# Kernel tuning notes

Measured on AMD Instinct MI355X. Metric: run time of the kernel, lower is better.

Reference implementation:

```python
import jax, jax.numpy as jnp
import numpy as np

VOCAB = 41      # len(MOL_DICT) + 1
EMB = 512       # EMBEDDING_SIZE
HID = 1024
B, T = 128, 256


def setup_inputs() -> dict:
    key = jax.random.key(0)
    ks = jax.random.split(key, 8)
    x = jax.random.randint(ks[0], (B, T), 0, VOCAB)
    # realistic prefix padding mask: True for valid tokens, False for padding
    lengths = jax.random.randint(ks[1], (B,), T // 4, T + 1)
    padding_mask = jnp.arange(T)[None, :] < lengths[:, None]
    s = 0.05
    emb_table = jax.random.normal(ks[2], (VOCAB, EMB), jnp.float32) * s
    gru_kernel = jax.random.normal(ks[3], (EMB, 3 * HID), jnp.float32) * s
    gru_rec_kernel = jax.random.normal(ks[4], (HID, 3 * HID), jnp.float32) * s
    gru_bias = jax.random.normal(ks[5], (2, 3 * HID), jnp.float32) * s
    dense_w = jax.random.normal(ks[6], (HID, VOCAB), jnp.float32) * s
    dense_b = jnp.zeros((VOCAB,), jnp.float32)
    return {"x": x, "padding_mask": padding_mask, "emb_table": emb_table,
            "gru_kernel": gru_kernel, "gru_rec_kernel": gru_rec_kernel,
            "gru_bias": gru_bias, "dense_w": dense_w, "dense_b": dense_b}


def _gru_scan(x_proj_t, mask_t, rec_kernel, rec_bias):
    # x_proj_t: [T, B, 3H] precomputed input projections; mask_t: [T, B] bool
    def step(h, inp):
        xp, m = inp                      # xp: [B, 3H], m: [B]
        rec = h @ rec_kernel + rec_bias  # [B, 3H]  (reset_after=True)
        xz, xr, xh = jnp.split(xp, 3, axis=-1)
        rz, rr, rh = jnp.split(rec, 3, axis=-1)
        z = jax.nn.sigmoid(xz + rz)
        r = jax.nn.sigmoid(xr + rr)
        hh = jnp.tanh(xh + r * rh)
        h_new = z * h + (1.0 - z) * hh
        # masked steps carry previous state/output forward (keras semantics)
        h = jnp.where(m[:, None], h_new, h)
        return h, h

    h0 = jnp.zeros((x_proj_t.shape[1], HID), x_proj_t.dtype)
    _, outs = jax.lax.scan(step, h0, (x_proj_t, mask_t))
    return outs  # [T, B, H]


def reference(x, padding_mask, emb_table, gru_kernel, gru_rec_kernel,
              gru_bias, dense_w, dense_b):
    xe = emb_table[x]                              # [B, T, E]
    x_proj = xe @ gru_kernel + gru_bias[0]         # [B, T, 3H]
    outs = _gru_scan(jnp.transpose(x_proj, (1, 0, 2)),
                     jnp.transpose(padding_mask, (1, 0)),
                     gru_rec_kernel, gru_bias[1])  # [T, B, H]
    h = jnp.transpose(outs, (1, 0, 2))             # [B, T, H]
    logits = h @ dense_w + dense_b                 # [B, T, VOCAB]
    return logits
```

## Files before the change

### kernel.cpp

```cpp
#include <hip/hip_runtime.h>
#include <stdint.h>
#include <stddef.h>

#define VOCAB 41
#define EMB   512
#define HID   1024
#define H3    3072
#define BB    128
#define TT    256
#define BT    (BB*TT)
#define NSLOT 8
#define SLOT_U64 32768

typedef unsigned short u16;
typedef _Float16 half_t;
typedef half_t f16x8 __attribute__((ext_vector_type(8)));
typedef float f32x4 __attribute__((ext_vector_type(4)));
typedef unsigned long long u64;
typedef u64 u64x2 __attribute__((ext_vector_type(2)));

__device__ __forceinline__ float bf2f(u16 u) {
  return __uint_as_float(((uint32_t)u) << 16);
}
__device__ __forceinline__ u16 f2bf(float f) {
  uint32_t x = __float_as_uint(f);
  return (u16)((x + 0x7FFFu + ((x >> 16) & 1u)) >> 16);
}
__device__ __forceinline__ u16 f2h_bits(float f) {
  half_t h = (half_t)f;
  return __builtin_bit_cast(u16, h);
}
__device__ __forceinline__ float sigmoidf_(float x) {
  return 1.0f / (1.0f + __expf(-x));
}
__device__ __forceinline__ float tanh_fast(float x) {
  return 1.0f - 2.0f / (__expf(2.0f * x) + 1.0f);
}
__device__ __forceinline__ u64 aload64(const u64* p) {
  return __hip_atomic_load(p, __ATOMIC_RELAXED, __HIP_MEMORY_SCOPE_AGENT);
}
__device__ __forceinline__ void astore64(u64* p, u64 v) {
  __hip_atomic_store(p, v, __ATOMIC_RELAXED, __HIP_MEMORY_SCOPE_AGENT);
}
__device__ __forceinline__ void poll_flags8(const int* flc, int idx, int target) {
  int cap = 0;
  while (true) {
    int v = __hip_atomic_load(flc + idx * 16, __ATOMIC_RELAXED,
                              __HIP_MEMORY_SCOPE_AGENT);
    if (__ballot(v < target) == 0ULL) break;
    __builtin_amdgcn_s_sleep(1);
    if (++cap > (1 << 16)) break;
  }
}


__global__ void detect_kernel(const u16* __restrict__ raw, int* __restrict__ flag) {
  __shared__ int s[256];
  int tid = threadIdx.x, cnt = 0;
  for (int i = tid; i < 4096; i += 256) {
    int e = (raw[i] >> 7) & 0xFF;
    if (e >= 132) cnt++;
  }
  s[tid] = cnt; __syncthreads();
  if (tid == 0) {
    int tot = 0;
    for (int i = 0; i < 256; i++) tot += s[i];
    *flag = (tot > 4) ? 1 : 0;
  }
}

__global__ void conv_kernel(const void* __restrict__ src, float* __restrict__ dst,
                            int n, const int* __restrict__ flag) {
  int i = blockIdx.x * 256 + threadIdx.x;
  if (i >= n) return;
  if (*flag) dst[i] = ((const float*)src)[i];
  else       dst[i] = bf2f(((const u16*)src)[i]);
}

__global__ void tokm_kernel(const int* __restrict__ x,
                            const unsigned char* __restrict__ m,
                            int* __restrict__ tokm) {
  int i = blockIdx.x * 256 + threadIdx.x;
  unsigned char b0 = m[0], b1 = m[1];
  bool t;
  if (b0 == 1) {
    if (b1 != 0) t = (m[i] != 0);
    else         t = (((const int*)m)[i] != 0);
  } else if (b0 == 0x80) {
    t = (((const u16*)m)[i] != 0);
  } else {
    t = (((const float*)m)[i] != 0.0f);
  }
  tokm[i] = x[i] | (t ? 0 : 0x80000000);
}

__global__ __launch_bounds__(256) void proj_kernel(
    const void* __restrict__ emb, const void* __restrict__ gk,
    const float* __restrict__ gbf, float* __restrict__ P,
    const int* __restrict__ flag) {
  int v = blockIdx.x / (H3 / 256);
  int j = (blockIdx.x % (H3 / 256)) * 256 + threadIdx.x;
  float acc = gbf[j];
  if (*flag) {
    const float* e = (const float*)emb + v * EMB;
    const float* g = (const float*)gk;
    for (int k = 0; k < EMB; ++k) acc = fmaf(e[k], g[k * H3 + j], acc);
  } else {
    const u16* e = (const u16*)emb + v * EMB;
    const u16* g = (const u16*)gk;
    for (int k = 0; k < EMB; ++k) acc = fmaf(bf2f(e[k]), bf2f(g[k * H3 + j]), acc);
  }
  P[v * H3 + j] = acc;
}

__global__ void p2_kernel(const float* __restrict__ P, const float* __restrict__ gbf,
                          float* __restrict__ P2) {
  int gc = blockIdx.x;
  int v = threadIdx.x;
  if (v >= VOCAB) return;
  float val = P[v * H3 + gc];
  if (gc < 2048) val += gbf[H3 + gc];
  P2[gc * VOCAB + v] = val;
}

__global__ void pack_wimg_kernel(const void* __restrict__ src, u16* __restrict__ img,
                                 const int* __restrict__ flag) {
  int idx = blockIdx.x * 256 + threadIdx.x;
  int j = idx & 7;
  int t1 = idx >> 3;
  int lane = t1 & 63;
  int t2 = t1 >> 6;
  int c = t2 % 6;
  int t3 = t2 / 6;
  int ks = t3 & 31;
  int ds = t3 >> 5;
  int g = c >> 1, dh = c & 1;
  int k = ks * 32 + (lane >> 4) * 8 + j;
  int col = g * 1024 + ds * 32 + dh * 16 + (lane & 15);
  float val;
  if (*flag) val = ((const float*)src)[(size_t)k * H3 + col];
  else       val = bf2f(((const u16*)src)[(size_t)k * H3 + col]);
  img[idx] = f2h_bits(val);
}

__global__ void pack_dimg_kernel(const void* __restrict__ src, u16* __restrict__ img,
                                 const int* __restrict__ flag) {
  int idx = blockIdx.x * 256 + threadIdx.x;
  int j = idx & 7;
  int t1 = idx >> 3;
  int lane = t1 & 63;
  int t2 = t1 >> 6;
  int ct = t2 % 3;
  int ks = t2 / 3;
  int k = ks * 32 + (lane >> 4) * 8 + j;
  int v = ct * 16 + (lane & 15);
  float val = 0.0f;
  if (v < VOCAB) {
    if (*flag) val = ((const float*)src)[(size_t)k * VOCAB + v];
    else       val = bf2f(((const u16*)src)[(size_t)k * VOCAB + v]);
  }
  img[idx] = f2h_bits(val);
}

__global__ __launch_bounds__(256, 1) void gru_persist(
    const uint4* __restrict__ Wimg, const int* __restrict__ tokm,
    const float* __restrict__ P2, const float* __restrict__ gbf,
    u64* __restrict__ exch, u16* __restrict__ Hout,
    int* __restrict__ flags) {
  int bid = blockIdx.x;
  int gt = bid & 7, ds = bid >> 3;
  int tid = threadIdx.x;
  int w = tid >> 6, lane = tid & 63;

  __shared__ float red[4][64][25];
  __shared__ u16 tr[512];
  __shared__ float Pl[3][32][41];
  __shared__ int tokL[16 * 259];

  f16x8 breg[6][8];
  {
    const uint4* wsrc = Wimg + (size_t)ds * (32 * 6) * 64 + lane;
    #pragma unroll
    for (int k8 = 0; k8 < 8; ++k8)
      #pragma unroll
      for (int c = 0; c < 6; ++c)
        breg[c][k8] = __builtin_bit_cast(f16x8, wsrc[((w * 8 + k8) * 6 + c) * 64]);
  }

  for (int i = tid; i < 3 * 32 * VOCAB; i += 256) {
    int v = i % VOCAB;
    int t1 = i / VOCAB;
    int di = t1 & 31, g = t1 >> 5;
    Pl[g][di][v] = P2[(size_t)(g * 1024 + ds * 32 + di) * VOCAB + v];
  }
  for (int i = tid; i < 16 * 256; i += 256) {
    int rr = i >> 8, cc = i & 255;
    tokL[rr * 259 + cc] = tokm[gt * 4096 + i];
  }

  int row = tid >> 4, dimb = tid & 15;
  int lane_src = (row >> 2) * 16 + dimb;
  int rg = row & 3;
  float b1h0 = gbf[H3 + 2048 + ds * 32 + dimb];
  float b1h1 = gbf[H3 + 2048 + ds * 32 + dimb + 16];
  float hc0 = 0.f, hc1 = 0.f;
  int* flc = flags + gt * 512;
  int widx = w * 8 + (lane & 7);
  __syncthreads();

  for (int t = 0; t < TT; ++t) {
    if (t > 0) poll_flags8(flc, widx, t);

    const u64* abase = exch + (size_t)(t & 7) * SLOT_U64 + gt * 4096 +
                       (w * 8) * 128 + lane * 2;
    u64 av[16];
    #pragma unroll
    for (int i = 0; i < 8; ++i) {
      av[2 * i]     = aload64(abase + i * 128);
      av[2 * i + 1] = aload64(abase + i * 128 + 1);
    }
    f32x4 acc[6];
    #pragma unroll
    for (int c = 0; c < 6; ++c) acc[c] = (f32x4){0.f, 0.f, 0.f, 0.f};
    #pragma unroll
    for (int k8 = 0; k8 < 8; ++k8) {
      u64x2 pair; pair.x = av[2 * k8]; pair.y = av[2 * k8 + 1];
      f16x8 a = __builtin_bit_cast(f16x8, pair);
      #pragma unroll
      for (int c = 0; c < 6; ++c)
        acc[c] = __builtin_amdgcn_mfma_f32_16x16x32_f16(a, breg[c][k8], acc[c], 0, 0, 0);
    }

    {
      float* q = red[w][lane];
      #pragma unroll
      for (int c = 0; c < 6; ++c)
        #pragma unroll
        for (int r = 0; r < 4; ++r) q[c * 4 + r] = acc[c][r];
    }
    __syncthreads();

    {
      int tm = tokL[row * 259 + t];
      int tok = tm & 0xFFFF;
      #pragma unroll
      for (int dh = 0; dh < 2; ++dh) {
        float a0 = 0.f, a1 = 0.f, a2 = 0.f;
        #pragma unroll
        for (int ww = 0; ww < 4; ++ww) {
          const float* q = red[ww][lane_src];
          a0 += q[(0 * 2 + dh) * 4 + rg];
          a1 += q[(1 * 2 + dh) * 4 + rg];
          a2 += q[(2 * 2 + dh) * 4 + rg];
        }
        int dglob = dimb + dh * 16;
        float z  = sigmoidf_(Pl[0][dglob][tok] + a0);
        float r_ = sigmoidf_(Pl[1][dglob][tok] + a1);
        float b1h = dh ? b1h1 : b1h0;
        float hh = tanh_fast(Pl[2][dglob][tok] + r_ * (a2 + b1h));
        float h = dh ? hc1 : hc0;
        if (tm >= 0) h = z * h + (1.0f - z) * hh;
        if (dh) hc1 = h; else hc0 = h;
        tr[(dglob >> 3) * 128 + row * 8 + (dglob & 7)] = f2h_bits(h);
      }
    }
    __syncthreads();

    if (w == 0) {
      u64 v0 = ((const u64*)tr)[lane];
      u64 v1 = ((const u64*)tr)[lane + 64];
      u64* ebase = exch + (size_t)((t + 1) & 7) * SLOT_U64 + gt * 4096 +
                   ds * 128;
      astore64(ebase + lane, v0);
      astore64(ebase + 64 + lane, v1);
      __atomic_signal_fence(__ATOMIC_SEQ_CST);
      __builtin_amdgcn_s_waitcnt(0);
      __atomic_signal_fence(__ATOMIC_SEQ_CST);
      if (lane == 0)
        __hip_atomic_fetch_add(flc + ds * 16, 1, __ATOMIC_RELAXED,
                               __HIP_MEMORY_SCOPE_AGENT);
      {
        int quad = lane >> 4, mm = lane & 15;
        uint4 hv = ((const uint4*)tr)[lane];
        int b = gt * 16 + mm;
        size_t idx = ((size_t)(b * 16 + (t >> 4)) * 32 + ds) * 64 +
                     quad * 16 + (t & 15);
        ((uint4*)Hout)[idx] = hv;
      }
    }
  }
}

__global__ __launch_bounds__(256) void dense_mfma(
    const u16* __restrict__ HoutImg, const uint4* __restrict__ dimg,
    const float* __restrict__ dbf, void* __restrict__ out,
    const int* __restrict__ flag) {
  __shared__ uint4 Bl[48 * 64];
  int tid = threadIdx.x;
  int w = tid >> 6, lane = tid & 63;
  int quad = lane >> 4, vi = lane & 15;
  int gt0 = blockIdx.x * 8 + w * 2;

  f32x4 acc[2][3];
  #pragma unroll
  for (int i = 0; i < 2; ++i)
    #pragma unroll
    for (int c = 0; c < 3; ++c) acc[i][c] = (f32x4){0.f, 0.f, 0.f, 0.f};

  for (int half = 0; half < 2; ++half) {
    for (int i = tid; i < 48 * 64; i += 256) Bl[i] = dimg[half * 48 * 64 + i];
    __syncthreads();
    #pragma unroll
    for (int ks16 = 0; ks16 < 16; ++ks16) {
      int ks = half * 16 + ks16;
      f16x8 a0 = __builtin_bit_cast(
          f16x8, ((const uint4*)HoutImg)[((size_t)gt0 * 32 + ks) * 64 + lane]);
      f16x8 a1 = __builtin_bit_cast(
          f16x8, ((const uint4*)HoutImg)[(((size_t)gt0 + 1) * 32 + ks) * 64 + lane]);
      #pragma unroll
      for (int c = 0; c < 3; ++c) {
        f16x8 bf = __builtin_bit_cast(f16x8, Bl[(ks16 * 3 + c) * 64 + lane]);
        acc[0][c] = __builtin_amdgcn_mfma_f32_16x16x32_f16(a0, bf, acc[0][c], 0, 0, 0);
        acc[1][c] = __builtin_amdgcn_mfma_f32_16x16x32_f16(a1, bf, acc[1][c], 0, 0, 0);
      }
    }
    __syncthreads();
  }

  int isf = *flag;
  #pragma unroll
  for (int i = 0; i < 2; ++i) {
    #pragma unroll
    for (int c = 0; c < 3; ++c) {
      int v = c * 16 + vi;
      if (v >= VOCAB) continue;
      float bias = dbf[v];
      #pragma unroll
      for (int rg = 0; rg < 4; ++rg) {
        size_t bt = (size_t)(gt0 + i) * 16 + quad * 4 + rg;
        float val = acc[i][c][rg] + bias;
        if (isf) ((float*)out)[bt * VOCAB + v] = val;
        else     ((u16*)out)[bt * VOCAB + v] = f2bf(val);
      }
    }
  }
}


extern "C" void kernel_launch(void* const* d_in, const int* in_sizes, int n_in,
                              void* d_out, int out_size, void* d_ws, size_t ws_size,
                              hipStream_t stream) {
  const int* x            = (const int*)d_in[0];
  const unsigned char* mk = (const unsigned char*)d_in[1];

  char* ws = (char*)d_ws;
  int*   flag  = (int*)(ws + 0);
  float* dbf   = (float*)(ws + 4 * 1024);
  float* gbf   = (float*)(ws + 8 * 1024);
  int*   flags = (int*)(ws + 32 * 1024);
  int*   tokm  = (int*)(ws + 64 * 1024);
  u16*   dimg  = (u16*)(ws + 192 * 1024);
  float* P     = (float*)(ws + 288 * 1024);
  float* P2    = (float*)(ws + 800 * 1024);
  u64*   exch  = (u64*)(ws + 1312 * 1024);
  u16*   Wimg  = (u16*)(ws + 3456 * 1024);
  u16*   Hout  = (u16*)(ws + 10 * 1024 * 1024);

  detect_kernel<<<1, 256, 0, stream>>>((const u16*)d_in[4], flag);
  conv_kernel<<<(2 * H3 + 255) / 256, 256, 0, stream>>>(d_in[5], gbf, 2 * H3, flag);
  conv_kernel<<<1, 256, 0, stream>>>(d_in[7], dbf, VOCAB, flag);
  tokm_kernel<<<BT / 256, 256, 0, stream>>>(x, mk, tokm);
  proj_kernel<<<VOCAB * (H3 / 256), 256, 0, stream>>>(d_in[2], d_in[3], gbf, P, flag);
  p2_kernel<<<H3, 64, 0, stream>>>(P, gbf, P2);
  pack_wimg_kernel<<<(32 * 32 * 6 * 64 * 8) / 256, 256, 0, stream>>>(d_in[4], Wimg, flag);
  pack_dimg_kernel<<<(32 * 3 * 64 * 8) / 256, 256, 0, stream>>>(d_in[6], dimg, flag);
  hipMemsetAsync(flags, 0, 16 * 1024, stream);
  hipMemsetAsync(exch, 0, SLOT_U64 * 8, stream);

  gru_persist<<<256, 256, 0, stream>>>((const uint4*)Wimg, tokm, P2, gbf,
                                       exch, Hout, flags);
  dense_mfma<<<256, 256, 0, stream>>>(Hout, (const uint4*)dimg, dbf, d_out, flag);
}
```

Measured before the change: 983.4 us.

## Replace flag counters with step-tagged exchange words in persistent GRU

```diff
diff --git a/kernel.cpp b/kernel.cpp
--- a/kernel.cpp
+++ b/kernel.cpp
@@ -9,15 +9,15 @@
 #define BB    128
 #define TT    256
 #define BT    (BB*TT)
-#define NSLOT 8
-#define SLOT_U64 32768
+#define NSLOT 4
+#define SLOT_U32 (8*32*512)
 
 typedef unsigned short u16;
+typedef uint32_t u32;
 typedef _Float16 half_t;
 typedef half_t f16x8 __attribute__((ext_vector_type(8)));
 typedef float f32x4 __attribute__((ext_vector_type(4)));
-typedef unsigned long long u64;
-typedef u64 u64x2 __attribute__((ext_vector_type(2)));
+typedef u32 u32x4 __attribute__((ext_vector_type(4)));
 
 __device__ __forceinline__ float bf2f(u16 u) {
   return __uint_as_float(((uint32_t)u) << 16);
@@ -35,22 +35,6 @@
 }
 __device__ __forceinline__ float tanh_fast(float x) {
   return 1.0f - 2.0f / (__expf(2.0f * x) + 1.0f);
-}
-__device__ __forceinline__ u64 aload64(const u64* p) {
-  return __hip_atomic_load(p, __ATOMIC_RELAXED, __HIP_MEMORY_SCOPE_AGENT);
-}
-__device__ __forceinline__ void astore64(u64* p, u64 v) {
-  __hip_atomic_store(p, v, __ATOMIC_RELAXED, __HIP_MEMORY_SCOPE_AGENT);
-}
-__device__ __forceinline__ void poll_flags8(const int* flc, int idx, int target) {
-  int cap = 0;
-  while (true) {
-    int v = __hip_atomic_load(flc + idx * 16, __ATOMIC_RELAXED,
-                              __HIP_MEMORY_SCOPE_AGENT);
-    if (__ballot(v < target) == 0ULL) break;
-    __builtin_amdgcn_s_sleep(1);
-    if (++cap > (1 << 16)) break;
-  }
 }
 
 
@@ -165,15 +149,14 @@
 __global__ __launch_bounds__(256, 1) void gru_persist(
     const uint4* __restrict__ Wimg, const int* __restrict__ tokm,
     const float* __restrict__ P2, const float* __restrict__ gbf,
-    u64* __restrict__ exch, u16* __restrict__ Hout,
-    int* __restrict__ flags) {
+    u32* __restrict__ exch, u16* __restrict__ Hout) {
   int bid = blockIdx.x;
   int gt = bid & 7, ds = bid >> 3;
   int tid = threadIdx.x;
   int w = tid >> 6, lane = tid & 63;
 
   __shared__ float red[4][64][25];
-  __shared__ u16 tr[512];
+  __shared__ __align__(16) u16 tr[512];
   __shared__ float Pl[3][32][41];
   __shared__ int tokL[16 * 259];
 
@@ -204,28 +187,59 @@
   float b1h0 = gbf[H3 + 2048 + ds * 32 + dimb];
   float b1h1 = gbf[H3 + 2048 + ds * 32 + dimb + 16];
   float hc0 = 0.f, hc1 = 0.f;
-  int* flc = flags + gt * 512;
-  int widx = w * 8 + (lane & 7);
   __syncthreads();
 
+  u32x4 d[16];
   for (int t = 0; t < TT; ++t) {
-    if (t > 0) poll_flags8(flc, widx, t);
-
-    const u64* abase = exch + (size_t)(t & 7) * SLOT_U64 + gt * 4096 +
-                       (w * 8) * 128 + lane * 2;
-    u64 av[16];
-    #pragma unroll
-    for (int i = 0; i < 8; ++i) {
-      av[2 * i]     = aload64(abase + i * 128);
-      av[2 * i + 1] = aload64(abase + i * 128 + 1);
-    }
+    const u32* slotb = exch + (size_t)(t & (NSLOT - 1)) * SLOT_U32;
+    {
+      const u32* sp = slotb + (size_t)(gt * 32 + (w * 8 + (lane & 7))) * 512 + 511;
+      int cap = 0;
+      while (true) {
+        u32 v = __hip_atomic_load(sp, __ATOMIC_RELAXED, __HIP_MEMORY_SCOPE_AGENT);
+        if (__ballot((v >> 16) != (u32)t) == 0ULL) break;
+        __builtin_amdgcn_s_sleep(1);
+        if (++cap > (1 << 16)) break;
+      }
+    }
+    {
+      const u32* abase = slotb + (size_t)(gt * 32 + w * 8) * 512 + lane * 8;
+      int cap = 0;
+      while (true) {
+        #pragma unroll
+        for (int i = 0; i < 8; ++i) {
+          asm volatile("global_load_dwordx4 %0, %2, off sc1\n\t"
+                       "global_load_dwordx4 %1, %2, off offset:16 sc1"
+                       : "=&v"(d[2 * i]), "=&v"(d[2 * i + 1])
+                       : "v"(abase + (size_t)i * 512) : "memory");
+        }
+        asm volatile("s_waitcnt vmcnt(0)" ::: "memory");
+        __builtin_amdgcn_sched_barrier(0);
+        u32 want = ((u32)t) << 16, bad = 0;
+        #pragma unroll
+        for (int i = 0; i < 16; ++i) {
+          u32x4 q = d[i];
+          bad |= (q.x ^ want) | (q.y ^ want) | (q.z ^ want) | (q.w ^ want);
+        }
+        bad &= 0xFFFF0000u;
+        if (__ballot(bad != 0) == 0ULL) break;
+        __builtin_amdgcn_s_sleep(1);
+        if (++cap > (1 << 16)) break;
+      }
+    }
+
     f32x4 acc[6];
     #pragma unroll
     for (int c = 0; c < 6; ++c) acc[c] = (f32x4){0.f, 0.f, 0.f, 0.f};
     #pragma unroll
     for (int k8 = 0; k8 < 8; ++k8) {
-      u64x2 pair; pair.x = av[2 * k8]; pair.y = av[2 * k8 + 1];
-      f16x8 a = __builtin_bit_cast(f16x8, pair);
+      u32x4 lo = d[2 * k8], hi = d[2 * k8 + 1];
+      u32x4 pk;
+      pk.x = (lo.y << 16) | (lo.x & 0xFFFFu);
+      pk.y = (lo.w << 16) | (lo.z & 0xFFFFu);
+      pk.z = (hi.y << 16) | (hi.x & 0xFFFFu);
+      pk.w = (hi.w << 16) | (hi.z & 0xFFFFu);
+      f16x8 a = __builtin_bit_cast(f16x8, pk);
       #pragma unroll
       for (int c = 0; c < 6; ++c)
         acc[c] = __builtin_amdgcn_mfma_f32_16x16x32_f16(a, breg[c][k8], acc[c], 0, 0, 0);
@@ -267,25 +281,24 @@
     __syncthreads();
 
     if (w == 0) {
-      u64 v0 = ((const u64*)tr)[lane];
-      u64 v1 = ((const u64*)tr)[lane + 64];
-      u64* ebase = exch + (size_t)((t + 1) & 7) * SLOT_U64 + gt * 4096 +
-                   ds * 128;
-      astore64(ebase + lane, v0);
-      astore64(ebase + 64 + lane, v1);
-      __atomic_signal_fence(__ATOMIC_SEQ_CST);
-      __builtin_amdgcn_s_waitcnt(0);
-      __atomic_signal_fence(__ATOMIC_SEQ_CST);
-      if (lane == 0)
-        __hip_atomic_fetch_add(flc + ds * 16, 1, __ATOMIC_RELAXED,
-                               __HIP_MEMORY_SCOPE_AGENT);
+      u32x4 tr4 = ((const u32x4*)tr)[lane];
+      u32 tag1 = ((u32)(t + 1)) << 16;
+      u32x4 o0, o1;
+      o0.x = tag1 | (tr4.x & 0xFFFFu); o0.y = tag1 | (tr4.x >> 16);
+      o0.z = tag1 | (tr4.y & 0xFFFFu); o0.w = tag1 | (tr4.y >> 16);
+      o1.x = tag1 | (tr4.z & 0xFFFFu); o1.y = tag1 | (tr4.z >> 16);
+      o1.z = tag1 | (tr4.w & 0xFFFFu); o1.w = tag1 | (tr4.w >> 16);
+      u32* eb = exch + (size_t)((t + 1) & (NSLOT - 1)) * SLOT_U32 +
+                (size_t)(gt * 32 + ds) * 512 + lane * 8;
+      asm volatile("global_store_dwordx4 %0, %1, off sc1\n\t"
+                   "global_store_dwordx4 %0, %2, off offset:16 sc1"
+                   :: "v"(eb), "v"(o0), "v"(o1) : "memory");
       {
         int quad = lane >> 4, mm = lane & 15;
-        uint4 hv = ((const uint4*)tr)[lane];
         int b = gt * 16 + mm;
         size_t idx = ((size_t)(b * 16 + (t >> 4)) * 32 + ds) * 64 +
                      quad * 16 + (t & 15);
-        ((uint4*)Hout)[idx] = hv;
+        ((u32x4*)Hout)[idx] = tr4;
       }
     }
   }
@@ -357,12 +370,11 @@
   int*   flag  = (int*)(ws + 0);
   float* dbf   = (float*)(ws + 4 * 1024);
   float* gbf   = (float*)(ws + 8 * 1024);
-  int*   flags = (int*)(ws + 32 * 1024);
   int*   tokm  = (int*)(ws + 64 * 1024);
   u16*   dimg  = (u16*)(ws + 192 * 1024);
   float* P     = (float*)(ws + 288 * 1024);
   float* P2    = (float*)(ws + 800 * 1024);
-  u64*   exch  = (u64*)(ws + 1312 * 1024);
+  u32*   exch  = (u32*)(ws + 1312 * 1024);
   u16*   Wimg  = (u16*)(ws + 3456 * 1024);
   u16*   Hout  = (u16*)(ws + 10 * 1024 * 1024);
 
@@ -374,10 +386,9 @@
   p2_kernel<<<H3, 64, 0, stream>>>(P, gbf, P2);
   pack_wimg_kernel<<<(32 * 32 * 6 * 64 * 8) / 256, 256, 0, stream>>>(d_in[4], Wimg, flag);
   pack_dimg_kernel<<<(32 * 3 * 64 * 8) / 256, 256, 0, stream>>>(d_in[6], dimg, flag);
-  hipMemsetAsync(flags, 0, 16 * 1024, stream);
-  hipMemsetAsync(exch, 0, SLOT_U64 * 8, stream);
+  hipMemsetAsync(exch, 0, (size_t)NSLOT * SLOT_U32 * 4, stream);
 
   gru_persist<<<256, 256, 0, stream>>>((const uint4*)Wimg, tokm, P2, gbf,
-                                       exch, Hout, flags);
+                                       exch, Hout);
   dense_mfma<<<256, 256, 0, stream>>>(Hout, (const uint4*)dimg, dbf, d_out, flag);
 }
```

Measured after the change: 1.153 ms. 1.17x slower.
